# Performance work log

Hardware: AMD Instinct MI355X
Metric: run time of the kernel (lower is better)

Reference implementation:

```python
import jax, jax.numpy as jnp
import numpy as np

B, T = 1, 1024
V, C, H, L = 50304, 768, 12, 6
K = C // H              # 64, d_head
F = int(C * 3.5) // 32 * 32   # 2688, d_ffn
GN_EPS = 6.4e-4


def _layernorm(x, wb, eps=1e-5):
    mu = x.mean(-1, keepdims=True)
    var = jnp.var(x, axis=-1, keepdims=True)
    return (x - mu) * jax.lax.rsqrt(var + eps) * wb[0] + wb[1]


def _groupnorm(x, wb):  # x: [N, C], groups of size K per head
    xg = x.reshape(-1, H, K)
    mu = xg.mean(-1, keepdims=True)
    var = jnp.var(xg, axis=-1, keepdims=True)
    xg = (xg - mu) * jax.lax.rsqrt(var + GN_EPS)
    return xg.reshape(-1, C) * wb[0] + wb[1]


def _lerp(a, b, w):  # torch.lerp(a, b, w) = a + (b - a) * w
    return a + (b - a) * w


def _shift(x):  # token-shift with zero initial state (fresh LayerState)
    return jnp.concatenate([jnp.zeros_like(x[:, :1]), x[:, :-1]], axis=1)


def _layer(x, p):
    (tm_ln, tm_ts, Wr, Wk, Wv, Wg, Wo, bonus, decay, tm_gn,
     cm_ln, cm_ts, Win, Wout, cWg) = p
    # ---- time mixer ----
    xn = _layernorm(x, tm_ln)
    xp = _shift(xn)
    r = (_lerp(xp, xn, tm_ts[0]) @ Wr).reshape(B, T, H, K)
    k = (_lerp(xp, xn, tm_ts[1]) @ Wk).reshape(B, T, H, K)
    v = (_lerp(xp, xn, tm_ts[2]) @ Wv).reshape(B, T, H, K)
    g = _lerp(xp, xn, tm_ts[3]) @ Wg
    w = jnp.exp(-jnp.exp(decay))  # [H, K] per-channel decay

    def wkv_step(kv, rkv):  # kv: [B,H,K,V]
        r_t, k_t, v_t = rkv  # each [B,H,K]
        a = k_t[..., :, None] * v_t[..., None, :]          # outer product kv_t
        out = jnp.einsum('bhk,bhkv->bhv', r_t, kv + a * bonus[..., None])
        return kv * w[..., None] + a, out

    kv0 = jnp.zeros((B, H, K, K), x.dtype)
    kv_final, out = jax.lax.scan(
        wkv_step, kv0,
        (r.transpose(1, 0, 2, 3), k.transpose(1, 0, 2, 3),
         v.transpose(1, 0, 2, 3)))
    out = out.transpose(1, 0, 2, 3).reshape(B, T, C)
    out = _groupnorm(out.reshape(B * T, C), tm_gn).reshape(B, T, C)
    x = x + (out * jax.nn.silu(g)) @ Wo
    # ---- channel mixer ----
    xn = _layernorm(x, cm_ln)
    xp = _shift(xn)
    h = jnp.square(jax.nn.relu(_lerp(xp, xn, cm_ts[0]) @ Win))
    x = x + (h @ Wout) * jax.nn.sigmoid(_lerp(xp, xn, cm_ts[1]) @ cWg)
    return x, kv_final


def _forward(tokens, embed, embed_ln, tm_ln, tm_ts, tm_Wr, tm_Wk, tm_Wv,
             tm_Wg, tm_Wo, tm_bonus, tm_decay, tm_gn, cm_ln, cm_ts, cm_Win,
             cm_Wout, cm_Wg, head_ln, unembed):
    x = _layernorm(embed[tokens], embed_ln)
    stacked = (tm_ln, tm_ts, tm_Wr, tm_Wk, tm_Wv, tm_Wg, tm_Wo, tm_bonus,
               tm_decay, tm_gn, cm_ln, cm_ts, cm_Win, cm_Wout, cm_Wg)
    x, _ = jax.lax.scan(_layer, x, stacked)  # scan over the L layers
    return _layernorm(x, head_ln) @ unembed  # logits [B, T, V]


def setup_inputs() -> dict:
    key = jax.random.key(0)
    ks = iter(jax.random.split(key, 48))

    def rn(shape, s=0.02):
        return s * jax.random.normal(next(ks), shape, jnp.float32)

    def ln(pre=()):  # stacked (weight, bias) of a LayerNorm/GroupNorm
        return jnp.stack([1.0 + rn(pre + (C,)), rn(pre + (C,))], axis=len(pre))

    return {
        'tokens': jax.random.randint(next(ks), (B, T), 0, V),
        'embed': rn((V, C)),
        'embed_ln': ln(),
        'tm_ln': ln((L,)),
        'tm_ts': jax.random.uniform(next(ks), (L, 4, C), jnp.float32),
        'tm_Wr': rn((L, C, C)),
        'tm_Wk': rn((L, C, C)),
        'tm_Wv': rn((L, C, C)),
        'tm_Wg': rn((L, C, C)),
        'tm_Wo': rn((L, C, C)),
        'tm_bonus': rn((L, H, K), 0.5),
        'tm_decay': rn((L, H, K), 0.5),
        'tm_gn': ln((L,)),
        'cm_ln': ln((L,)),
        'cm_ts': jax.random.uniform(next(ks), (L, 2, C), jnp.float32),
        'cm_Win': rn((L, C, F)),
        'cm_Wout': rn((L, F, C)),
        'cm_Wg': rn((L, C, C)),
        'head_ln': ln(),
        'unembed': rn((C, V)),
    }


def reference(tokens, embed, embed_ln, tm_ln, tm_ts, tm_Wr, tm_Wk, tm_Wv,
              tm_Wg, tm_Wo, tm_bonus, tm_decay, tm_gn, cm_ln, cm_ts, cm_Win,
              cm_Wout, cm_Wg, head_ln, unembed):
    return _forward(tokens, embed, embed_ln, tm_ln, tm_ts, tm_Wr, tm_Wk,
                    tm_Wv, tm_Wg, tm_Wo, tm_bonus, tm_decay, tm_gn, cm_ln,
                    cm_ts, cm_Win, cm_Wout, cm_Wg, head_ln, unembed)
```

## Files before the change

kernel.cpp:

```cpp
#include <hip/hip_runtime.h>
#include <hip/hip_bf16.h>

#define T_LEN 1024
#define CDIM  768
#define HNUM  12
#define KDIM  64
#define LNUM  6
#define FDIM  2688
#define VDIM  50304
#define NCH   16
#define LCH   64

#define WSZ   (CDIM * CDIM)
#define WIN_OFF  (6 * WSZ)
#define WOUT_OFF (WIN_OFF + CDIM * FDIM)
#define WBUF_ELEMS (WOUT_OFF + FDIM * CDIM)

typedef __attribute__((ext_vector_type(4))) float f32x4;
typedef __attribute__((ext_vector_type(8))) short s16x8;

__device__ __forceinline__ ushort f2bf(float f) {
    union { float fv; unsigned u; } v; v.fv = f;
    unsigned r = v.u + 0x7fffu + ((v.u >> 16) & 1u);
    return (ushort)(r >> 16);
}

__device__ __forceinline__ void gload_lds16(const ushort* g, ushort* l) {
    __builtin_amdgcn_global_load_lds(
        (const __attribute__((address_space(1))) void*)g,
        (__attribute__((address_space(3))) void*)l, 16, 0, 0);
}

template <int N_>
__device__ __forceinline__ void wait_vm() {
    if constexpr (N_ == 0)       asm volatile("s_waitcnt vmcnt(0)" ::: "memory");
    else if constexpr (N_ == 4)  asm volatile("s_waitcnt vmcnt(4)" ::: "memory");
    else if constexpr (N_ == 6)  asm volatile("s_waitcnt vmcnt(6)" ::: "memory");
    else if constexpr (N_ == 8)  asm volatile("s_waitcnt vmcnt(8)" ::: "memory");
    else if constexpr (N_ == 12) asm volatile("s_waitcnt vmcnt(12)" ::: "memory");
    else                         asm volatile("s_waitcnt vmcnt(16)" ::: "memory");
}
__device__ __forceinline__ void barrier_asm() {
    asm volatile("s_barrier" ::: "memory");
}

__device__ __forceinline__ void trans_pair(const float* __restrict__ in,
        ushort* __restrict__ out, int R, int C, int tk, int tn0) {
    __shared__ float t0[64][65], t1[64][65];
    int tid = threadIdx.x;
    int r = tid >> 4, c4 = (tid & 15) << 2;
    int k0 = tk << 6, n0 = tn0 << 7, n1 = n0 + 64;
    float4 va[4], vb[4];
    #pragma unroll
    for (int j = 0; j < 4; j++)
        va[j] = *(const float4*)&in[(size_t)(k0 + r + j * 16) * C + n0 + c4];
    #pragma unroll
    for (int j = 0; j < 4; j++)
        vb[j] = *(const float4*)&in[(size_t)(k0 + r + j * 16) * C + n1 + c4];
    #pragma unroll
    for (int j = 0; j < 4; j++) {
        int rr = r + j * 16;
        t0[rr][c4 + 0] = va[j].x; t0[rr][c4 + 1] = va[j].y;
        t0[rr][c4 + 2] = va[j].z; t0[rr][c4 + 3] = va[j].w;
        t1[rr][c4 + 0] = vb[j].x; t1[rr][c4 + 1] = vb[j].y;
        t1[rr][c4 + 2] = vb[j].z; t1[rr][c4 + 3] = vb[j].w;
    }
    __syncthreads();
    #pragma unroll
    for (int j = 0; j < 4; j++) {
        int n = r + j * 16;
        ushort4 u0, u1;
        u0.x = f2bf(t0[c4 + 0][n]); u0.y = f2bf(t0[c4 + 1][n]);
        u0.z = f2bf(t0[c4 + 2][n]); u0.w = f2bf(t0[c4 + 3][n]);
        *(ushort4*)&out[(size_t)(n0 + n) * R + k0 + c4] = u0;
        u1.x = f2bf(t1[c4 + 0][n]); u1.y = f2bf(t1[c4 + 1][n]);
        u1.z = f2bf(t1[c4 + 2][n]); u1.w = f2bf(t1[c4 + 3][n]);
        *(ushort4*)&out[(size_t)(n1 + n) * R + k0 + c4] = u1;
    }
}

__device__ __forceinline__ void trans_tile(const float* __restrict__ in,
        ushort* __restrict__ out, int R, int C, int tk, int tn) {
    __shared__ float tile[64][65];
    int tid = threadIdx.x;
    int r = tid >> 4, c4 = (tid & 15) << 2;
    int k0 = tk << 6, n0 = tn << 6;
    #pragma unroll
    for (int j = 0; j < 4; j++) {
        int rr = r + j * 16;
        float4 f = *(const float4*)&in[(size_t)(k0 + rr) * C + n0 + c4];
        tile[rr][c4 + 0] = f.x; tile[rr][c4 + 1] = f.y;
        tile[rr][c4 + 2] = f.z; tile[rr][c4 + 3] = f.w;
    }
    __syncthreads();
    #pragma unroll
    for (int j = 0; j < 4; j++) {
        int n = r + j * 16;
        ushort4 u;
        u.x = f2bf(tile[c4 + 0][n]);
        u.y = f2bf(tile[c4 + 1][n]);
        u.z = f2bf(tile[c4 + 2][n]);
        u.w = f2bf(tile[c4 + 3][n]);
        *(ushort4*)&out[(size_t)(n0 + n) * R + k0 + c4] = u;
    }
}

__global__ __launch_bounds__(256)
void k_trans(const float* __restrict__ in, ushort* __restrict__ out, int R, int C) {
    trans_tile(in, out, R, C, blockIdx.y, blockIdx.x);
}

__device__ __forceinline__ void conv_layer_pair(int t,
        const float* p0, const float* p1, const float* p2, const float* p3,
        const float* p4, const float* p5, const float* pWin, const float* pWout,
        ushort* wl) {
    const float* in; ushort* out; int R, C, tk, tnp;
    if (t < 432) {
        int mi = t / 72, tt = t % 72;
        switch (mi) {
            case 0: in = p0; break; case 1: in = p1; break;
            case 2: in = p2; break; case 3: in = p3; break;
            case 4: in = p4; break; default: in = p5; break;
        }
        out = wl + (size_t)mi * WSZ; R = 768; C = 768;
        tk = tt / 6; tnp = tt % 6;
    } else if (t < 684) {
        int tt = t - 432;
        in = pWin; out = wl + WIN_OFF; R = 768; C = 2688;
        tk = tt / 21; tnp = tt % 21;
    } else {
        int tt = t - 684;
        in = pWout; out = wl + WOUT_OFF; R = 2688; C = 768;
        tk = tt / 6; tnp = tt % 6;
    }
    trans_pair(in, out, R, C, tk, tnp);
}

__global__ __launch_bounds__(256)
void k_conv_layer(const float* p0, const float* p1, const float* p2,
                  const float* p3, const float* p4, const float* p5,
                  const float* pWin, const float* pWout, ushort* wl) {
    conv_layer_pair(blockIdx.x, p0, p1, p2, p3, p4, p5, pWin, pWout, wl);
}

__global__ __launch_bounds__(256)
void k_conv_all(const float* Wr, const float* Wk, const float* Wv,
                const float* Wg, const float* Wo, const float* Wcg,
                const float* Win, const float* Wout, const float* unemb,
                ushort* wbuf, ushort* ubuf) {
    int b = blockIdx.x;
    if (b < 6 * 936) {
        int l = b / 936, t = b % 936;
        conv_layer_pair(t,
            Wr + (size_t)l * WSZ, Wk + (size_t)l * WSZ, Wv + (size_t)l * WSZ,
            Wg + (size_t)l * WSZ, Wo + (size_t)l * WSZ, Wcg + (size_t)l * WSZ,
            Win + (size_t)l * CDIM * FDIM, Wout + (size_t)l * FDIM * CDIM,
            wbuf + (size_t)l * WBUF_ELEMS);
    } else {
        int t = b - 6 * 936;
        int tk = t / 393, tnp = t % 393;
        trans_pair(unemb, ubuf, CDIM, VDIM, tk, tnp);
    }
}

__global__ __launch_bounds__(256)
void k_ln_bf(const float* __restrict__ x, const float* __restrict__ wb,
             ushort* __restrict__ out) {
    int t = blockIdx.x, tid = threadIdx.x;
    float v[3]; float s = 0.f, s2 = 0.f;
    #pragma unroll
    for (int j = 0; j < 3; j++) {
        v[j] = x[(size_t)t * CDIM + tid + j * 256];
        s += v[j]; s2 += v[j] * v[j];
    }
    #pragma unroll
    for (int m = 32; m; m >>= 1) { s += __shfl_xor(s, m); s2 += __shfl_xor(s2, m); }
    __shared__ float rs[4], rq[4];
    int w = tid >> 6;
    if ((tid & 63) == 0) { rs[w] = s; rq[w] = s2; }
    __syncthreads();
    s = rs[0] + rs[1] + rs[2] + rs[3];
    s2 = rq[0] + rq[1] + rq[2] + rq[3];
    float mu = s * (1.f / CDIM);
    float inv = rsqrtf(s2 * (1.f / CDIM) - mu * mu + 1e-5f);
    #pragma unroll
    for (int j = 0; j < 3; j++) {
        int c = tid + j * 256;
        out[(size_t)t * CDIM + c] = f2bf((v[j] - mu) * inv * wb[c] + wb[CDIM + c]);
    }
}

__global__ __launch_bounds__(256)
void k_embed_ln(const int* __restrict__ tok, const float* __restrict__ embed,
                const float* __restrict__ wb, float* __restrict__ xout) {
    int t = blockIdx.x, tid = threadIdx.x;
    const float* row = embed + (size_t)tok[t] * CDIM;
    float v[3]; float s = 0.f, s2 = 0.f;
    #pragma unroll
    for (int j = 0; j < 3; j++) {
        v[j] = row[tid + j * 256]; s += v[j]; s2 += v[j] * v[j];
    }
    #pragma unroll
    for (int m = 32; m; m >>= 1) { s += __shfl_xor(s, m); s2 += __shfl_xor(s2, m); }
    __shared__ float rs[4], rq[4];
    int w = tid >> 6;
    if ((tid & 63) == 0) { rs[w] = s; rq[w] = s2; }
    __syncthreads();
    s = rs[0] + rs[1] + rs[2] + rs[3];
    s2 = rq[0] + rq[1] + rq[2] + rq[3];
    float mu = s * (1.f / CDIM);
    float inv = rsqrtf(s2 * (1.f / CDIM) - mu * mu + 1e-5f);
    #pragma unroll
    for (int j = 0; j < 3; j++) {
        int c = tid + j * 256;
        xout[(size_t)t * CDIM + c] = (v[j] - mu) * inv * wb[c] + wb[CDIM + c];
    }
}

template <int NM>
__global__ __launch_bounds__(256)
void k_lnlerp(const float* __restrict__ x, const float* __restrict__ lnw,
              const float* __restrict__ ts, ushort* __restrict__ mix) {
    int t = blockIdx.x, tid = threadIdx.x;
    bool has = (t > 0);
    float vb[3], va[3];
    float sb = 0.f, qb = 0.f, sa = 0.f, qa = 0.f;
    #pragma unroll
    for (int j = 0; j < 3; j++) {
        int c = tid + j * 256;
        vb[j] = x[(size_t)t * CDIM + c];
        sb += vb[j]; qb += vb[j] * vb[j];
        va[j] = has ? x[(size_t)(t - 1) * CDIM + c] : 0.f;
        sa += va[j]; qa += va[j] * va[j];
    }
    #pragma unroll
    for (int m = 32; m; m >>= 1) {
        sb += __shfl_xor(sb, m); qb += __shfl_xor(qb, m);
        sa += __shfl_xor(sa, m); qa += __shfl_xor(qa, m);
    }
    __shared__ float r0[4], r1[4], r2[4], r3[4];
    int w = tid >> 6;
    if ((tid & 63) == 0) { r0[w] = sb; r1[w] = qb; r2[w] = sa; r3[w] = qa; }
    __syncthreads();
    sb = r0[0] + r0[1] + r0[2] + r0[3]; qb = r1[0] + r1[1] + r1[2] + r1[3];
    sa = r2[0] + r2[1] + r2[2] + r2[3]; qa = r3[0] + r3[1] + r3[2] + r3[3];
    float mub = sb * (1.f / CDIM);
    float invb = rsqrtf(qb * (1.f / CDIM) - mub * mub + 1e-5f);
    float mua = sa * (1.f / CDIM);
    float inva = rsqrtf(qa * (1.f / CDIM) - mua * mua + 1e-5f);
    #pragma unroll
    for (int j = 0; j < 3; j++) {
        int c = tid + j * 256;
        float wgt = lnw[c], bia = lnw[CDIM + c];
        float xb = (vb[j] - mub) * invb * wgt + bia;
        float xa = has ? (va[j] - mua) * inva * wgt + bia : 0.f;
        #pragma unroll
        for (int m = 0; m < NM; m++) {
            float tv = ts[m * CDIM + c];
            mix[((size_t)m * T_LEN + t) * CDIM + c] = f2bf(xa + (xb - xa) * tv);
        }
    }
}

template <int BM, int BN, int EPI, int NBUF>
__device__ __forceinline__ void gemm_body(
        const ushort* __restrict__ A, const ushort* __restrict__ Bt,
        float* __restrict__ Cf, ushort* __restrict__ Cb,
        const float* __restrict__ resid, const float* __restrict__ gate,
        int N, int K, int mb, int nb, ushort* Al, ushort* Bl) {
    const int tid = threadIdx.x, lane = tid & 63, wave = tid >> 6;
    constexpr int WM = BM / 2, WN = BN / 2, FM = WM / 16, FN = WN / 16;
    const int wm = (wave >> 1) * WM, wn = (wave & 1) * WN;
    constexpr int AR = (BM * 8) / 256;
    constexpr int BR = (BN * 8) / 256;
    constexpr int LD = AR + BR;

    auto stage = [&](int buf, int kt) {
        int k0 = kt << 6;
        #pragma unroll
        for (int r = 0; r < AR; r++) {
            int slot = tid + r * 256;
            int row = slot >> 3, g = slot & 7;
            int gk = ((g ^ (row & 7)) << 3);
            gload_lds16(A + (size_t)(mb + row) * K + k0 + gk,
                        &Al[buf * BM * 64 + slot * 8]);
        }
        #pragma unroll
        for (int r = 0; r < BR; r++) {
            int slot = tid + r * 256;
            int row = slot >> 3, g = slot & 7;
            int gk = ((g ^ (row & 7)) << 3);
            gload_lds16(Bt + (size_t)(nb + row) * K + k0 + gk,
                        &Bl[buf * BN * 64 + slot * 8]);
        }
    };

    f32x4 acc[FM][FN];
    #pragma unroll
    for (int i = 0; i < FM; i++)
        #pragma unroll
        for (int j = 0; j < FN; j++) acc[i][j] = (f32x4)0.f;

    const int nt = K >> 6;
    #pragma unroll
    for (int p = 0; p < NBUF; p++) stage(p, p);
    int cur = 0;
    for (int t = 0; t < nt; t++) {
        int ahead = nt - 1 - t;
        if constexpr (NBUF == 3) {
            if (ahead >= 2)      wait_vm<2 * LD>();
            else if (ahead == 1) wait_vm<LD>();
            else                 wait_vm<0>();
        } else {
            if (ahead >= 1)      wait_vm<LD>();
            else                 wait_vm<0>();
        }
        barrier_asm();
        const ushort* Ab = &Al[cur * BM * 64];
        const ushort* Bb = &Bl[cur * BN * 64];
        const int kq = lane >> 4, ln15 = lane & 15;
        #pragma unroll
        for (int s = 0; s < 2; s++) {
            s16x8 af[FM], bfr[FN];
            #pragma unroll
            for (int i = 0; i < FM; i++) {
                int row = wm + i * 16 + ln15;
                int g = (s * 4 + kq) ^ (row & 7);
                af[i] = *(const s16x8*)&Ab[row * 64 + g * 8];
            }
            #pragma unroll
            for (int j = 0; j < FN; j++) {
                int row = wn + j * 16 + ln15;
                int g = (s * 4 + kq) ^ (row & 7);
                bfr[j] = *(const s16x8*)&Bb[row * 64 + g * 8];
            }
            #pragma unroll
            for (int i = 0; i < FM; i++)
                #pragma unroll
                for (int j = 0; j < FN; j++)
                    acc[i][j] = __builtin_amdgcn_mfma_f32_16x16x32_bf16(
                        af[i], bfr[j], acc[i][j], 0, 0, 0);
        }
        barrier_asm();
        if (t + NBUF < nt) stage(cur, t + NBUF);
        cur = (cur + 1 == NBUF) ? 0 : cur + 1;
    }
    #pragma unroll
    for (int i = 0; i < FM; i++) {
        int rbase = mb + wm + i * 16 + (lane >> 4) * 4;
        #pragma unroll
        for (int j = 0; j < FN; j++) {
            int col = nb + wn + j * 16 + (lane & 15);
            #pragma unroll
            for (int r = 0; r < 4; r++) {
                size_t idx = (size_t)(rbase + r) * N + col;
                float vv = acc[i][j][r];
                if constexpr (EPI == 0) {
                    Cf[idx] = vv;
                } else if constexpr (EPI == 1) {
                    Cf[idx] = resid[idx] + vv;
                } else if constexpr (EPI == 2) {
                    float z = vv > 0.f ? vv * vv : 0.f;
                    Cb[idx] = f2bf(z);
                } else {
                    float gv = gate[idx];
                    Cf[idx] = resid[idx] + vv / (1.f + __expf(-gv));
                }
            }
        }
    }
}

template <int BM, int BN, int EPI, bool BATCH>
__global__ __launch_bounds__(256)
void k_gemm_std(const ushort* __restrict__ A, const ushort* __restrict__ Bt,
                float* __restrict__ Cf, ushort* __restrict__ Cb,
                const float* __restrict__ resid, const float* __restrict__ gate,
                int N, int K) {
    __shared__ __align__(16) ushort Al[2 * BM * 64];
    __shared__ __align__(16) ushort Bl[2 * BN * 64];
    if constexpr (BATCH) {
        int z = blockIdx.z;
        A  += (size_t)z * T_LEN * CDIM;
        Bt += (size_t)z * CDIM * CDIM;
        Cf += (size_t)z * T_LEN * CDIM;
    }
    gemm_body<BM, BN, EPI, 2>(A, Bt, Cf, Cb, resid, gate, N, K,
                              blockIdx.y * BM, blockIdx.x * BN, Al, Bl);
}

__global__ __launch_bounds__(256)
void k_gemm_head(const ushort* __restrict__ A, const ushort* __restrict__ Bt,
                 float* __restrict__ C) {
    __shared__ __align__(16) ushort Al[2 * 128 * 64];
    __shared__ __align__(16) ushort Bl[2 * 128 * 64];
    int id = blockIdx.x;
    int xcd = id & 7, slot = id >> 3;
    int mb = slot & 7, nbl = slot >> 3;
    int nb = nbl * 8 + xcd;
    if (nb >= VDIM / 128) return;
    gemm_body<128, 128, 0, 2>(A, Bt, C, nullptr, nullptr, nullptr,
                              VDIM, CDIM, mb * 128, nb * 128, Al, Bl);
}

__global__ __launch_bounds__(256)
void k_cmix(const ushort* __restrict__ mix, const ushort* __restrict__ wl,
            ushort* __restrict__ hb, float* __restrict__ gcm) {
    __shared__ __align__(16) ushort Al[2 * 128 * 64];
    __shared__ __align__(16) ushort Bl[2 * 64 * 64];
    int bx = blockIdx.x, mb = blockIdx.y * 128;
    if (bx < FDIM / 64) {
        gemm_body<128, 64, 2, 2>(mix, wl + WIN_OFF, nullptr, hb, nullptr, nullptr,
                                 FDIM, CDIM, mb, bx * 64, Al, Bl);
    } else {
        gemm_body<128, 64, 0, 2>(mix + (size_t)T_LEN * CDIM, wl + 5 * WSZ, gcm,
                                 nullptr, nullptr, nullptr, CDIM, CDIM, mb,
                                 (bx - FDIM / 64) * 64, Al, Bl);
    }
}

__global__ __launch_bounds__(256)
void k_wkv1(const float* __restrict__ kb, const float* __restrict__ vb,
            const float* __restrict__ decay, float* __restrict__ Stil) {
    int c = blockIdx.x / HNUM, h = blockIdx.x % HNUM;
    __shared__ float kl[4096], vl[4096], wsh[64];
    int tid = threadIdx.x;
    for (int idx = tid; idx < 4096; idx += 256) {
        int j = idx >> 6, cc = idx & 63;
        size_t g = (size_t)(c * LCH + j) * CDIM + h * 64 + cc;
        kl[idx] = kb[g]; vl[idx] = vb[g];
    }
    if (tid < 64) wsh[tid] = expf(-expf(decay[h * 64 + tid]));
    __syncthreads();
    int k = tid >> 2, v0 = (tid & 3) * 16;
    float w = wsh[k], f = 1.f;
    float s[16];
    #pragma unroll
    for (int i = 0; i < 16; i++) s[i] = 0.f;
    for (int j = 63; j >= 0; --j) {
        float kw = kl[j * 64 + k] * f;
        #pragma unroll
        for (int i = 0; i < 16; i++) s[i] += kw * vl[j * 64 + v0 + i];
        f *= w;
    }
    float* dst = Stil + ((size_t)(c * HNUM + h) << 12) + k * 64 + v0;
    #pragma unroll
    for (int i = 0; i < 16; i++) dst[i] = s[i];
}

__global__ __launch_bounds__(256)
void k_wkv23(const float* __restrict__ rb, const float* __restrict__ kb,
             const float* __restrict__ vb, const float* __restrict__ Stil,
             const float* __restrict__ decay, const float* __restrict__ bonus,
             const float* __restrict__ gate, const float* __restrict__ gnw,
             ushort* __restrict__ y) {
    int c = blockIdx.x / HNUM, h = blockIdx.x % HNUM;
    __shared__ float rl[4096], kl[4096], vl[4096];
    __shared__ float part[4][4096];
    __shared__ float wsh[64], bsh[64];
    int tid = threadIdx.x;
    for (int idx = tid; idx < 4096; idx += 256) {
        int j = idx >> 6, cc = idx & 63;
        size_t g = (size_t)(c * LCH + j) * CDIM + h * 64 + cc;
        rl[idx] = rb[g]; kl[idx] = kb[g]; vl[idx] = vb[g];
    }
    if (tid < 64) {
        wsh[tid] = expf(-expf(decay[h * 64 + tid]));
        bsh[tid] = bonus[h * 64 + tid];
    }
    __syncthreads();
    int v = tid & 63, kg = tid >> 6;
    float S[16], wr[16], br[16], w64[16];
    #pragma unroll
    for (int i = 0; i < 16; i++) {
        S[i] = 0.f;
        wr[i] = wsh[kg * 16 + i];
        br[i] = bsh[kg * 16 + i];
        float t2 = wr[i];
        t2 *= t2; t2 *= t2; t2 *= t2; t2 *= t2; t2 *= t2; t2 *= t2;
        w64[i] = t2;
    }
    for (int cc = 0; cc < c; cc++) {
        const float* sp = Stil + ((size_t)(cc * HNUM + h) << 12);
        #pragma unroll
        for (int i = 0; i < 16; i++)
            S[i] = S[i] * w64[i] + sp[(kg * 16 + i) * 64 + v];
    }
    for (int j = 0; j < 64; j++) {
        float vj = vl[j * 64 + v];
        const float4* kp = (const float4*)&kl[j * 64 + kg * 16];
        const float4* rp = (const float4*)&rl[j * 64 + kg * 16];
        float rsum = 0.f;
        #pragma unroll
        for (int qq = 0; qq < 4; qq++) {
            float4 k4 = kp[qq], r4 = rp[qq];
            const float* kf = (const float*)&k4;
            const float* rf = (const float*)&r4;
            #pragma unroll
            for (int e = 0; e < 4; e++) {
                int i = qq * 4 + e;
                float a = kf[e] * vj;
                rsum += rf[e] * (S[i] + a * br[i]);
                S[i] = S[i] * wr[i] + a;
            }
        }
        part[kg][j * 64 + v] = rsum;
    }
    __syncthreads();
    for (int jj = 0; jj < 16; jj++) {
        int j = kg * 16 + jj;
        float o = part[0][j * 64 + v] + part[1][j * 64 + v] +
                  part[2][j * 64 + v] + part[3][j * 64 + v];
        float s = o, s2 = o * o;
        #pragma unroll
        for (int m = 32; m; m >>= 1) { s += __shfl_xor(s, m); s2 += __shfl_xor(s2, m); }
        float mu = s * (1.f / 64.f);
        float var = s2 * (1.f / 64.f) - mu * mu;
        float xg = (o - mu) * rsqrtf(var + 6.4e-4f);
        int t = c * LCH + j, col = h * 64 + v;
        float gv = gate[(size_t)t * CDIM + col];
        float silu = gv / (1.f + __expf(-gv));
        y[(size_t)t * CDIM + col] = f2bf((xg * gnw[col] + gnw[CDIM + col]) * silu);
    }
}

extern "C" void kernel_launch(void* const* d_in, const int* in_sizes, int n_in,
                              void* d_out, int out_size, void* d_ws, size_t ws_size,
                              hipStream_t stream) {
    const int*   tok      = (const int*)d_in[0];
    const float* embed    = (const float*)d_in[1];
    const float* embed_ln = (const float*)d_in[2];
    const float* tm_ln    = (const float*)d_in[3];
    const float* tm_ts    = (const float*)d_in[4];
    const float* tm_Wr    = (const float*)d_in[5];
    const float* tm_Wk    = (const float*)d_in[6];
    const float* tm_Wv    = (const float*)d_in[7];
    const float* tm_Wg    = (const float*)d_in[8];
    const float* tm_Wo    = (const float*)d_in[9];
    const float* tm_bonus = (const float*)d_in[10];
    const float* tm_decay = (const float*)d_in[11];
    const float* tm_gn    = (const float*)d_in[12];
    const float* cm_ln    = (const float*)d_in[13];
    const float* cm_ts    = (const float*)d_in[14];
    const float* cm_Win   = (const float*)d_in[15];
    const float* cm_Wout  = (const float*)d_in[16];
    const float* cm_Wg    = (const float*)d_in[17];
    const float* head_ln  = (const float*)d_in[18];
    const float* unembed  = (const float*)d_in[19];
    float* out = (float*)d_out;

    const size_t TC = (size_t)T_LEN * CDIM;
    char* wp = (char*)d_ws;
    auto alloc = [&](size_t bytes) {
        char* p = wp; wp += (bytes + 255) & ~(size_t)255; return p;
    };
    float*  x    = (float*)alloc(TC * 4);
    ushort* mix  = (ushort*)alloc(4 * TC * 2);
    float*  rkvg = (float*)alloc(4 * TC * 4);
    float*  gcm  = (float*)alloc(TC * 4);
    ushort* y    = (ushort*)alloc(TC * 2);
    ushort* hb   = (ushort*)alloc((size_t)T_LEN * FDIM * 2);
    float*  Stil = (float*)alloc((size_t)NCH * HNUM * 4096 * 4);
    ushort* ubuf = (ushort*)alloc((size_t)CDIM * VDIM * 2);
    size_t fixed_bytes = (size_t)(wp - (char*)d_ws);
    const size_t per_layer = ((size_t)WBUF_ELEMS * 2 + 255) & ~(size_t)255;
    bool all6 = (fixed_bytes + 6 * per_layer) <= ws_size;
    ushort* wbuf = (ushort*)alloc(all6 ? 6 * per_layer : per_layer);
    if ((size_t)(wp - (char*)d_ws) > ws_size) return;

    if (all6) {
        k_conv_all<<<6 * 936 + 4716, 256, 0, stream>>>(
            tm_Wr, tm_Wk, tm_Wv, tm_Wg, tm_Wo, cm_Wg, cm_Win, cm_Wout,
            unembed, wbuf, ubuf);
    } else {
        k_trans<<<dim3(VDIM / 64, CDIM / 64), 256, 0, stream>>>(
            unembed, ubuf, CDIM, VDIM);
    }
    k_embed_ln<<<T_LEN, 256, 0, stream>>>(tok, embed, embed_ln, x);

    dim3 g64(CDIM / 64, T_LEN / 64);
    dim3 gQKVG(CDIM / 64, T_LEN / 128, 4);
    dim3 gCmix(FDIM / 64 + CDIM / 64, T_LEN / 128);

    for (int l = 0; l < LNUM; l++) {
        ushort* wl = all6 ? (ushort*)((char*)wbuf + (size_t)l * per_layer) : wbuf;
        if (!all6) {
            const size_t lo = (size_t)l * CDIM * CDIM;
            k_conv_layer<<<936, 256, 0, stream>>>(
                tm_Wr + lo, tm_Wk + lo, tm_Wv + lo, tm_Wg + lo, tm_Wo + lo,
                cm_Wg + lo, cm_Win + (size_t)l * CDIM * FDIM,
                cm_Wout + (size_t)l * FDIM * CDIM, wl);
        }
        const float* dec = tm_decay + (size_t)l * HNUM * KDIM;
        const float* bon = tm_bonus + (size_t)l * HNUM * KDIM;

        k_lnlerp<4><<<T_LEN, 256, 0, stream>>>(x, tm_ln + (size_t)l * 2 * CDIM,
                                               tm_ts + (size_t)l * 4 * CDIM, mix);
        k_gemm_std<128,64,0,true><<<gQKVG, 256, 0, stream>>>(
            mix, wl, rkvg, nullptr, nullptr, nullptr, CDIM, CDIM);
        k_wkv1<<<NCH * HNUM, 256, 0, stream>>>(rkvg + TC, rkvg + 2 * TC, dec, Stil);
        k_wkv23<<<NCH * HNUM, 256, 0, stream>>>(rkvg, rkvg + TC, rkvg + 2 * TC,
            Stil, dec, bon, rkvg + 3 * TC, tm_gn + (size_t)l * 2 * CDIM, y);
        k_gemm_std<64,64,1,false><<<g64, 256, 0, stream>>>(
            y, wl + 4 * WSZ, x, nullptr, x, nullptr, CDIM, CDIM);

        k_lnlerp<2><<<T_LEN, 256, 0, stream>>>(x, cm_ln + (size_t)l * 2 * CDIM,
                                               cm_ts + (size_t)l * 2 * CDIM, mix);
        k_cmix<<<gCmix, 256, 0, stream>>>(mix, wl, hb, gcm);
        k_gemm_std<64,64,3,false><<<g64, 256, 0, stream>>>(
            hb, wl + WOUT_OFF, x, nullptr, x, gcm, CDIM, FDIM);
    }

    k_ln_bf<<<T_LEN, 256, 0, stream>>>(x, head_ln, mix);
    k_gemm_head<<<3200, 256, 0, stream>>>(mix, ubuf, out);
}
```

Before: 969.0 us.

## Pre-pack weights into MFMA fragment layout and load B directly to registers

Weight conversion now writes bf16 weights in a fragment-major layout, so each lane can fetch its MFMA B operand with one contiguous 16-byte global load. The GEMM drops the B shared-memory tile and loads B straight into registers, double-buffered alongside the LDS-staged A tile in an unrolled two-stage loop. This removes B's LDS traffic and shared-memory footprint. In exchange it raises register pressure and relies on the loop assuming an even K-tile count.

```diff
diff --git a/kernel.cpp b/kernel.cpp
--- a/kernel.cpp
+++ b/kernel.cpp
@@ -34,7 +34,6 @@
 template <int N_>
 __device__ __forceinline__ void wait_vm() {
     if constexpr (N_ == 0)       asm volatile("s_waitcnt vmcnt(0)" ::: "memory");
-    else if constexpr (N_ == 4)  asm volatile("s_waitcnt vmcnt(4)" ::: "memory");
     else if constexpr (N_ == 6)  asm volatile("s_waitcnt vmcnt(6)" ::: "memory");
     else if constexpr (N_ == 8)  asm volatile("s_waitcnt vmcnt(8)" ::: "memory");
     else if constexpr (N_ == 12) asm volatile("s_waitcnt vmcnt(12)" ::: "memory");
@@ -42,6 +41,13 @@
 }
 __device__ __forceinline__ void barrier_asm() {
     asm volatile("s_barrier" ::: "memory");
+}
+
+__device__ __forceinline__ size_t frag_idx(int nn, int k, int K) {
+    int n16 = nn >> 4, ln15 = nn & 15;
+    int k64 = k >> 6, s = (k >> 5) & 1, kq = (k >> 3) & 3;
+    return ((size_t)(n16 * (K >> 6) + k64) * 2 + s) * 512 + (kq * 16 + ln15) * 8
+           + (k & 4);
 }
 
 __device__ __forceinline__ void trans_pair(const float* __restrict__ in,
@@ -72,10 +78,10 @@
         ushort4 u0, u1;
         u0.x = f2bf(t0[c4 + 0][n]); u0.y = f2bf(t0[c4 + 1][n]);
         u0.z = f2bf(t0[c4 + 2][n]); u0.w = f2bf(t0[c4 + 3][n]);
-        *(ushort4*)&out[(size_t)(n0 + n) * R + k0 + c4] = u0;
+        *(ushort4*)&out[frag_idx(n0 + n, k0 + c4, R)] = u0;
         u1.x = f2bf(t1[c4 + 0][n]); u1.y = f2bf(t1[c4 + 1][n]);
         u1.z = f2bf(t1[c4 + 2][n]); u1.w = f2bf(t1[c4 + 3][n]);
-        *(ushort4*)&out[(size_t)(n1 + n) * R + k0 + c4] = u1;
+        *(ushort4*)&out[frag_idx(n1 + n, k0 + c4, R)] = u1;
     }
 }
 
@@ -101,7 +107,7 @@
         u.y = f2bf(tile[c4 + 1][n]);
         u.z = f2bf(tile[c4 + 2][n]);
         u.w = f2bf(tile[c4 + 3][n]);
-        *(ushort4*)&out[(size_t)(n0 + n) * R + k0 + c4] = u;
+        *(ushort4*)&out[frag_idx(n0 + n, k0 + c4, R)] = u;
     }
 }
 
@@ -262,20 +268,24 @@
     }
 }
 
-template <int BM, int BN, int EPI, int NBUF>
+template <int BM, int BN, int EPI>
 __device__ __forceinline__ void gemm_body(
-        const ushort* __restrict__ A, const ushort* __restrict__ Bt,
+        const ushort* __restrict__ A, const ushort* __restrict__ Bf,
         float* __restrict__ Cf, ushort* __restrict__ Cb,
         const float* __restrict__ resid, const float* __restrict__ gate,
-        int N, int K, int mb, int nb, ushort* Al, ushort* Bl) {
+        int N, int K, int mb, int nb, ushort* Al) {
     const int tid = threadIdx.x, lane = tid & 63, wave = tid >> 6;
     constexpr int WM = BM / 2, WN = BN / 2, FM = WM / 16, FN = WN / 16;
     const int wm = (wave >> 1) * WM, wn = (wave & 1) * WN;
-    constexpr int AR = (BM * 8) / 256;
-    constexpr int BR = (BN * 8) / 256;
-    constexpr int LD = AR + BR;
-
-    auto stage = [&](int buf, int kt) {
+    constexpr int AR = BM / 32;
+    constexpr int LD = AR + 2 * FN;
+    const int kq = lane >> 4, ln15 = lane & 15;
+
+    const size_t bstride = (size_t)(K >> 6) * 2048;
+    const char* bbase = (const char*)Bf +
+        (size_t)((nb + wn) >> 4) * bstride + lane * 16;
+
+    auto stageA = [&](int buf, int kt) {
         int k0 = kt << 6;
         #pragma unroll
         for (int r = 0; r < AR; r++) {
@@ -285,15 +295,15 @@
             gload_lds16(A + (size_t)(mb + row) * K + k0 + gk,
                         &Al[buf * BM * 64 + slot * 8]);
         }
-        #pragma unroll
-        for (int r = 0; r < BR; r++) {
-            int slot = tid + r * 256;
-            int row = slot >> 3, g = slot & 7;
-            int gk = ((g ^ (row & 7)) << 3);
-            gload_lds16(Bt + (size_t)(nb + row) * K + k0 + gk,
-                        &Bl[buf * BN * 64 + slot * 8]);
-        }
     };
+    auto loadB = [&](s16x8 (&dst)[2][FN], int kt) {
+        const char* p = bbase + (size_t)kt * 2048;
+        #pragma unroll
+        for (int s = 0; s < 2; s++)
+            #pragma unroll
+            for (int j = 0; j < FN; j++)
+                dst[s][j] = *(const s16x8*)(p + (size_t)j * bstride + s * 1024);
+    };
 
     f32x4 acc[FM][FN];
     #pragma unroll
@@ -301,27 +311,10 @@
         #pragma unroll
         for (int j = 0; j < FN; j++) acc[i][j] = (f32x4)0.f;
 
-    const int nt = K >> 6;
-    #pragma unroll
-    for (int p = 0; p < NBUF; p++) stage(p, p);
-    int cur = 0;
-    for (int t = 0; t < nt; t++) {
-        int ahead = nt - 1 - t;
-        if constexpr (NBUF == 3) {
-            if (ahead >= 2)      wait_vm<2 * LD>();
-            else if (ahead == 1) wait_vm<LD>();
-            else                 wait_vm<0>();
-        } else {
-            if (ahead >= 1)      wait_vm<LD>();
-            else                 wait_vm<0>();
-        }
-        barrier_asm();
-        const ushort* Ab = &Al[cur * BM * 64];
-        const ushort* Bb = &Bl[cur * BN * 64];
-        const int kq = lane >> 4, ln15 = lane & 15;
+    auto compute = [&](const ushort* Ab, s16x8 (&bfr)[2][FN]) {
         #pragma unroll
         for (int s = 0; s < 2; s++) {
-            s16x8 af[FM], bfr[FN];
+            s16x8 af[FM];
             #pragma unroll
             for (int i = 0; i < FM; i++) {
                 int row = wm + i * 16 + ln15;
@@ -329,21 +322,30 @@
                 af[i] = *(const s16x8*)&Ab[row * 64 + g * 8];
             }
             #pragma unroll
-            for (int j = 0; j < FN; j++) {
-                int row = wn + j * 16 + ln15;
-                int g = (s * 4 + kq) ^ (row & 7);
-                bfr[j] = *(const s16x8*)&Bb[row * 64 + g * 8];
-            }
-            #pragma unroll
             for (int i = 0; i < FM; i++)
                 #pragma unroll
                 for (int j = 0; j < FN; j++)
                     acc[i][j] = __builtin_amdgcn_mfma_f32_16x16x32_bf16(
-                        af[i], bfr[j], acc[i][j], 0, 0, 0);
+                        af[i], bfr[s][j], acc[i][j], 0, 0, 0);
         }
+    };
+
+    const int nt = K >> 6;
+    s16x8 b0[2][FN], b1[2][FN];
+    stageA(0, 0); loadB(b0, 0);
+    stageA(1, 1); loadB(b1, 1);
+    for (int t = 0; t < nt; t += 2) {
+        wait_vm<LD>();
         barrier_asm();
-        if (t + NBUF < nt) stage(cur, t + NBUF);
-        cur = (cur + 1 == NBUF) ? 0 : cur + 1;
+        compute(Al, b0);
+        barrier_asm();
+        if (t + 2 < nt) { stageA(0, t + 2); loadB(b0, t + 2); }
+        if (t + 2 < nt) wait_vm<LD>();
+        else            wait_vm<0>();
+        barrier_asm();
+        compute(Al + BM * 64, b1);
+        barrier_asm();
+        if (t + 3 < nt) { stageA(1, t + 3); loadB(b1, t + 3); }
     }
     #pragma unroll
     for (int i = 0; i < FM; i++) {
@@ -373,49 +375,46 @@
 
 template <int BM, int BN, int EPI, bool BATCH>
 __global__ __launch_bounds__(256)
-void k_gemm_std(const ushort* __restrict__ A, const ushort* __restrict__ Bt,
+void k_gemm_std(const ushort* __restrict__ A, const ushort* __restrict__ Bf,
                 float* __restrict__ Cf, ushort* __restrict__ Cb,
                 const float* __restrict__ resid, const float* __restrict__ gate,
                 int N, int K) {
     __shared__ __align__(16) ushort Al[2 * BM * 64];
-    __shared__ __align__(16) ushort Bl[2 * BN * 64];
     if constexpr (BATCH) {
         int z = blockIdx.z;
         A  += (size_t)z * T_LEN * CDIM;
-        Bt += (size_t)z * CDIM * CDIM;
+        Bf += (size_t)z * CDIM * CDIM;
         Cf += (size_t)z * T_LEN * CDIM;
     }
-    gemm_body<BM, BN, EPI, 2>(A, Bt, Cf, Cb, resid, gate, N, K,
-                              blockIdx.y * BM, blockIdx.x * BN, Al, Bl);
-}
-
-__global__ __launch_bounds__(256)
-void k_gemm_head(const ushort* __restrict__ A, const ushort* __restrict__ Bt,
+    gemm_body<BM, BN, EPI>(A, Bf, Cf, Cb, resid, gate, N, K,
+                           blockIdx.y * BM, blockIdx.x * BN, Al);
+}
+
+__global__ __launch_bounds__(256)
+void k_gemm_head(const ushort* __restrict__ A, const ushort* __restrict__ Bf,
                  float* __restrict__ C) {
     __shared__ __align__(16) ushort Al[2 * 128 * 64];
-    __shared__ __align__(16) ushort Bl[2 * 128 * 64];
     int id = blockIdx.x;
     int xcd = id & 7, slot = id >> 3;
     int mb = slot & 7, nbl = slot >> 3;
     int nb = nbl * 8 + xcd;
     if (nb >= VDIM / 128) return;
-    gemm_body<128, 128, 0, 2>(A, Bt, C, nullptr, nullptr, nullptr,
-                              VDIM, CDIM, mb * 128, nb * 128, Al, Bl);
+    gemm_body<128, 128, 0>(A, Bf, C, nullptr, nullptr, nullptr,
+                           VDIM, CDIM, mb * 128, nb * 128, Al);
 }
 
 __global__ __launch_bounds__(256)
 void k_cmix(const ushort* __restrict__ mix, const ushort* __restrict__ wl,
             ushort* __restrict__ hb, float* __restrict__ gcm) {
     __shared__ __align__(16) ushort Al[2 * 128 * 64];
-    __shared__ __align__(16) ushort Bl[2 * 64 * 64];
     int bx = blockIdx.x, mb = blockIdx.y * 128;
     if (bx < FDIM / 64) {
-        gemm_body<128, 64, 2, 2>(mix, wl + WIN_OFF, nullptr, hb, nullptr, nullptr,
-                                 FDIM, CDIM, mb, bx * 64, Al, Bl);
+        gemm_body<128, 64, 2>(mix, wl + WIN_OFF, nullptr, hb, nullptr, nullptr,
+                              FDIM, CDIM, mb, bx * 64, Al);
     } else {
-        gemm_body<128, 64, 0, 2>(mix + (size_t)T_LEN * CDIM, wl + 5 * WSZ, gcm,
-                                 nullptr, nullptr, nullptr, CDIM, CDIM, mb,
-                                 (bx - FDIM / 64) * 64, Al, Bl);
+        gemm_body<128, 64, 0>(mix + (size_t)T_LEN * CDIM, wl + 5 * WSZ, gcm,
+                              nullptr, nullptr, nullptr, CDIM, CDIM, mb,
+                              (bx - FDIM / 64) * 64, Al);
     }
 }
 
```

Result: faster. 893.0 us (-7.8%).
